# Kernel optimization log

Measured on AMD Instinct MI355X. Metric: run time of the kernel, lower is better.

The kernel has to match this reference:

```python
import jax, jax.numpy as jnp
import numpy as np

N_NODES = 50000
N_EDGES = 800000
IN_C = 128
HID = 128
OUT_C = 64
N_GRAPHS = 256


def setup_inputs() -> dict:
    key = jax.random.key(0)
    ks = jax.random.split(key, 12)
    x = jax.random.normal(ks[0], (N_NODES, IN_C), dtype=jnp.float32)
    edge_index = jax.random.randint(ks[1], (2, N_EDGES), 0, N_NODES, dtype=jnp.int32)
    batch = jnp.sort(jax.random.randint(ks[2], (N_NODES,), 0, N_GRAPHS, dtype=jnp.int32))
    def lin(k, fan_in, fan_out):
        bound = 1.0 / np.sqrt(fan_in)
        kw, kb = jax.random.split(k)
        W = jax.random.uniform(kw, (fan_in, fan_out), minval=-bound, maxval=bound, dtype=jnp.float32)
        b = jax.random.uniform(kb, (fan_out,), minval=-bound, maxval=bound, dtype=jnp.float32)
        return W, b
    W1a, b1a = lin(ks[3], IN_C, HID)
    W1b, b1b = lin(ks[4], HID, HID)
    W2a, b2a = lin(ks[5], HID, HID)
    W2b, b2b = lin(ks[6], HID, HID)
    Wl, bl = lin(ks[7], HID, OUT_C)
    return {"x": x, "edge_index": edge_index, "batch": batch,
            "W1a": W1a, "b1a": b1a, "W1b": W1b, "b1b": b1b,
            "W2a": W2a, "b2a": b2a, "W2b": W2b, "b2b": b2b,
            "Wl": Wl, "bl": bl}


def gin_conv(x, edge_index, Wa, ba, Wb, bb):
    # GINConv with eps=0: h_i = MLP(x_i + sum_{j->i} x_j)
    src, dst = edge_index[0], edge_index[1]
    agg = jax.ops.segment_sum(x[src], dst, num_segments=x.shape[0])  # [N, d]
    h = x + agg
    h = jax.nn.relu(h @ Wa + ba) @ Wb + bb
    return h


def reference(x, edge_index, batch, W1a, b1a, W1b, b1b, W2a, b2a, W2b, b2b, Wl, bl):
    h = gin_conv(x, edge_index, W1a, b1a, W1b, b1b)
    h = gin_conv(h, edge_index, W2a, b2a, W2b, b2b)
    # global mean pool over graphs in the batch
    sums = jax.ops.segment_sum(h, batch, num_segments=N_GRAPHS)          # [G, HID]
    cnts = jax.ops.segment_sum(jnp.ones((h.shape[0],), h.dtype), batch, num_segments=N_GRAPHS)
    pooled = sums / jnp.maximum(cnts, 1.0)[:, None]
    return pooled @ Wl + bl  # [G, OUT_C]
```

## Files before the change

kernel.cpp:

```cpp
#include <hip/hip_runtime.h>

constexpr int N  = 50000;
constexpr int E  = 800000;
constexpr int C  = 128;
constexpr int G  = 256;
constexpr int OC = 64;
constexpr int D  = 64;

constexpr int NBUCK = 196;
constexpr int BCAP  = 5120;
constexpr int EB = (E + 4095) / 4096;
constexpr int WB = 256;
constexpr int XB = (N * C / 8 + 255) / 256;
constexpr int GB = (N + 255) / 256;

typedef __attribute__((ext_vector_type(8))) short short8;
typedef __attribute__((ext_vector_type(4))) float f32x4;
typedef __attribute__((ext_vector_type(2))) float f32x2;

__device__ __forceinline__ unsigned int au(float f) { return __float_as_uint(f); }

__device__ __forceinline__ unsigned short f2bf(float f) {
    unsigned int u = au(f);
    u += 0x7fffu + ((u >> 16) & 1u);
    return (unsigned short)(u >> 16);
}
__device__ __forceinline__ unsigned int pack_bf16(float lo, float hi) {
    return ((au(hi) + 0x8000u) & 0xFFFF0000u) | ((au(lo) + 0x8000u) >> 16);
}

__device__ __forceinline__ void acc16(f32x2* a, uint4 v) {
    a[0] += __builtin_amdgcn_cvt_pk_f32_fp8((int)v.x, false);
    a[1] += __builtin_amdgcn_cvt_pk_f32_fp8((int)v.x, true);
    a[2] += __builtin_amdgcn_cvt_pk_f32_fp8((int)v.y, false);
    a[3] += __builtin_amdgcn_cvt_pk_f32_fp8((int)v.y, true);
    a[4] += __builtin_amdgcn_cvt_pk_f32_fp8((int)v.z, false);
    a[5] += __builtin_amdgcn_cvt_pk_f32_fp8((int)v.z, true);
    a[6] += __builtin_amdgcn_cvt_pk_f32_fp8((int)v.w, false);
    a[7] += __builtin_amdgcn_cvt_pk_f32_fp8((int)v.w, true);
}
__device__ __forceinline__ void set16(f32x2* a, uint4 v) {
    a[0] = __builtin_amdgcn_cvt_pk_f32_fp8((int)v.x, false);
    a[1] = __builtin_amdgcn_cvt_pk_f32_fp8((int)v.x, true);
    a[2] = __builtin_amdgcn_cvt_pk_f32_fp8((int)v.y, false);
    a[3] = __builtin_amdgcn_cvt_pk_f32_fp8((int)v.y, true);
    a[4] = __builtin_amdgcn_cvt_pk_f32_fp8((int)v.z, false);
    a[5] = __builtin_amdgcn_cvt_pk_f32_fp8((int)v.z, true);
    a[6] = __builtin_amdgcn_cvt_pk_f32_fp8((int)v.w, false);
    a[7] = __builtin_amdgcn_cvt_pk_f32_fp8((int)v.w, true);
}


__global__ __launch_bounds__(256) void build_prep_kernel(const int* __restrict__ src,
                                                         const int* __restrict__ dst,
                                                         int* __restrict__ bcount,
                                                         unsigned int* __restrict__ bucketbuf,
                                                         const float* __restrict__ W1a,
                                                         const float* __restrict__ W1b,
                                                         const float* __restrict__ W2a,
                                                         const float* __restrict__ W2b,
                                                         const float* __restrict__ x,
                                                         unsigned short* __restrict__ wt,
                                                         unsigned int* __restrict__ x8,
                                                         const int* __restrict__ batch,
                                                         int* __restrict__ gcnt) {
    int b = blockIdx.x;
    if (b < EB) {
        __shared__ int lcount[NBUCK];
        __shared__ int lbase[NBUCK];
        __shared__ int lcur[NBUCK];
        int tid = threadIdx.x;
        for (int i = tid; i < NBUCK; i += 256) { lcount[i] = 0; lcur[i] = 0; }
        __syncthreads();
        int e0 = b * 4096;
        int sv[16], dv[16];
#pragma unroll
        for (int i = 0; i < 16; ++i) {
            int e = e0 + i * 256 + tid;
            if (e < E) {
                sv[i] = src[e];
                dv[i] = dst[e];
                atomicAdd(&lcount[dv[i] >> 8], 1);
            } else {
                dv[i] = -1;
            }
        }
        __syncthreads();
        if (tid < NBUCK) {
            int c = lcount[tid];
            lbase[tid] = (c > 0) ? atomicAdd(&bcount[tid], c) : 0;
        }
        __syncthreads();
#pragma unroll
        for (int i = 0; i < 16; ++i) {
            if (dv[i] >= 0) {
                int bk = dv[i] >> 8;
                int pos = lbase[bk] + atomicAdd(&lcur[bk], 1);
                if (pos < BCAP)
                    bucketbuf[(size_t)bk * BCAP + pos] =
                        ((unsigned int)sv[i] << 16) | (unsigned int)(dv[i] & 255);
            }
        }
    } else if (b < EB + WB) {
        const float* Ws[4] = {W1a, W1b, W2a, W2b};
        int idx = (b - EB) * 256 + threadIdx.x;
        int which = idx >> 14;
        int el    = idx & 16383;
        int n = el >> 7, k = el & 127;
        wt[idx] = f2bf(Ws[which][k * 128 + n]);
    } else if (b < EB + WB + XB) {
        int idx = (b - EB - WB) * 256 + threadIdx.x;
        const float4* x4 = (const float4*)x;
        float4 v0 = x4[idx * 2];
        float4 v1 = x4[idx * 2 + 1];
        unsigned int lo = 0, hi = 0;
        lo = (unsigned int)__builtin_amdgcn_cvt_pk_fp8_f32(v0.x, v0.y, (int)lo, false);
        lo = (unsigned int)__builtin_amdgcn_cvt_pk_fp8_f32(v0.z, v0.w, (int)lo, true);
        hi = (unsigned int)__builtin_amdgcn_cvt_pk_fp8_f32(v1.x, v1.y, (int)hi, false);
        hi = (unsigned int)__builtin_amdgcn_cvt_pk_fp8_f32(v1.z, v1.w, (int)hi, true);
        ((uint2*)x8)[idx] = make_uint2(lo, hi);
    } else {
        __shared__ int h[G];
        int tid = threadIdx.x;
        h[tid] = 0;
        __syncthreads();
        int i = (b - EB - WB - XB) * 256 + tid;
        if (i < N) atomicAdd(&h[batch[i]], 1);
        __syncthreads();
        int c = h[tid];
        if (c > 0) atomicAdd(&gcnt[tid], c);
    }
}


__global__ __launch_bounds__(256) void bucket_fill_kernel(const int* __restrict__ bcount,
                                                          const unsigned int* __restrict__ bucketbuf,
                                                          unsigned short* __restrict__ ell,
                                                          int* __restrict__ deg) {
    __shared__ int lcur[256];
    int b = blockIdx.x;
    int tid = threadIdx.x;
    lcur[tid] = 0;
    __syncthreads();
    int cnt = min(bcount[b], BCAP);
    const unsigned int* buf = bucketbuf + (size_t)b * BCAP;
    int nbase = b << 8;
    for (int i = tid; i < cnt; i += 256) {
        unsigned int e = buf[i];
        int dlow = (int)(e & 255u);
        int s = (int)(e >> 16);
        int p = atomicAdd(&lcur[dlow], 1);
        if (p < D) ell[(size_t)p * N + nbase + dlow] = (unsigned short)s;
    }
    __syncthreads();
    int node = nbase + tid;
    if (node < N) deg[node] = lcur[tid];
}


__global__ __launch_bounds__(256) void conv_kernel(const unsigned char* __restrict__ Fg,
                                                   const int* __restrict__ deg,
                                                   const unsigned short* __restrict__ ell,
                                                   const unsigned short* __restrict__ WaT,
                                                   const float* __restrict__ ba,
                                                   const unsigned short* __restrict__ WbT,
                                                   const float* __restrict__ bb,
                                                   unsigned char* __restrict__ Hg8,
                                                   const int* __restrict__ batch,
                                                   float* __restrict__ gsum,
                                                   int outFp8) {
    constexpr int LD = 136;
    __shared__ short Xl[64 * LD];
    __shared__ short Wl[128 * LD];
    int tid  = threadIdx.x;
    int lane = tid & 63;
    int wave = tid >> 6;
    int row0 = blockIdx.x * 64;

    const short8* Wa8 = (const short8*)WaT;
#pragma unroll
    for (int i = tid; i < 2048; i += 256) {
        int r = i >> 4, c = i & 15;
        *((short8*)(Wl + r * LD) + c) = Wa8[i];
    }

    {
        int grp = tid >> 3;
        int l   = tid & 7;
        const uint4* F16 = (const uint4*)Fg;
#pragma unroll 1
        for (int pass = 0; pass < 2; ++pass) {
            int lr = pass * 32 + grp;
            int n  = row0 + lr;
            f32x2 a[8];
            if (n < N) {
                int dg = min(deg[n], D);
                const unsigned short* ecol = ell + n;
                set16(a, F16[(size_t)n * 8 + l]);
                int j = 0;
                if (dg >= 8) {
                    int i0 = ecol[0];
                    int i1 = ecol[(size_t)1 * N];
                    int i2 = ecol[(size_t)2 * N];
                    int i3 = ecol[(size_t)3 * N];
                    int i4 = ecol[(size_t)4 * N];
                    int i5 = ecol[(size_t)5 * N];
                    int i6 = ecol[(size_t)6 * N];
                    int i7 = ecol[(size_t)7 * N];
                    uint4 v0 = F16[(size_t)i0 * 8 + l];
                    uint4 v1 = F16[(size_t)i1 * 8 + l];
                    uint4 v2 = F16[(size_t)i2 * 8 + l];
                    uint4 v3 = F16[(size_t)i3 * 8 + l];
                    uint4 v4 = F16[(size_t)i4 * 8 + l];
                    uint4 v5 = F16[(size_t)i5 * 8 + l];
                    uint4 v6 = F16[(size_t)i6 * 8 + l];
                    uint4 v7 = F16[(size_t)i7 * 8 + l];
                    for (j = 8; j + 8 <= dg; j += 8) {
                        int t0 = ecol[(size_t)(j + 0) * N];
                        int t1 = ecol[(size_t)(j + 1) * N];
                        int t2 = ecol[(size_t)(j + 2) * N];
                        int t3 = ecol[(size_t)(j + 3) * N];
                        int t4 = ecol[(size_t)(j + 4) * N];
                        int t5 = ecol[(size_t)(j + 5) * N];
                        int t6 = ecol[(size_t)(j + 6) * N];
                        int t7 = ecol[(size_t)(j + 7) * N];
                        uint4 w0 = F16[(size_t)t0 * 8 + l];
                        uint4 w1 = F16[(size_t)t1 * 8 + l];
                        uint4 w2 = F16[(size_t)t2 * 8 + l];
                        uint4 w3 = F16[(size_t)t3 * 8 + l];
                        uint4 w4 = F16[(size_t)t4 * 8 + l];
                        uint4 w5 = F16[(size_t)t5 * 8 + l];
                        uint4 w6 = F16[(size_t)t6 * 8 + l];
                        uint4 w7 = F16[(size_t)t7 * 8 + l];
                        acc16(a, v0); acc16(a, v1); acc16(a, v2); acc16(a, v3);
                        acc16(a, v4); acc16(a, v5); acc16(a, v6); acc16(a, v7);
                        v0 = w0; v1 = w1; v2 = w2; v3 = w3;
                        v4 = w4; v5 = w5; v6 = w6; v7 = w7;
                    }
                    acc16(a, v0); acc16(a, v1); acc16(a, v2); acc16(a, v3);
                    acc16(a, v4); acc16(a, v5); acc16(a, v6); acc16(a, v7);
                }
                for (; j < dg; ++j) {
                    uint4 v = F16[(size_t)ecol[(size_t)j * N] * 8 + l];
                    acc16(a, v);
                }
            } else {
#pragma unroll
                for (int q = 0; q < 8; ++q) a[q] = (f32x2){0.f, 0.f};
            }
            uint4 o0, o1;
            o0.x = pack_bf16(a[0].x, a[0].y); o0.y = pack_bf16(a[1].x, a[1].y);
            o0.z = pack_bf16(a[2].x, a[2].y); o0.w = pack_bf16(a[3].x, a[3].y);
            o1.x = pack_bf16(a[4].x, a[4].y); o1.y = pack_bf16(a[5].x, a[5].y);
            o1.z = pack_bf16(a[6].x, a[6].y); o1.w = pack_bf16(a[7].x, a[7].y);
            uint4* xp = (uint4*)(Xl + lr * LD + l * 16);
            xp[0] = o0;
            xp[1] = o1;
        }
    }

    int mw = wave >> 1, nw = wave & 1;
    int lid = lane & 15, quad = lane >> 4;

    f32x4 acc[2][4];
#pragma unroll
    for (int nt = 0; nt < 4; ++nt) {
        float b = ba[nw * 64 + nt * 16 + lid];
        acc[0][nt] = (f32x4){b, b, b, b};
        acc[1][nt] = (f32x4){b, b, b, b};
    }
    __syncthreads();

#pragma unroll
    for (int ks = 0; ks < 4; ++ks) {
        short8 a0 = *(const short8*)(Xl + (mw * 32 + lid) * LD + ks * 32 + quad * 8);
        short8 a1 = *(const short8*)(Xl + (mw * 32 + 16 + lid) * LD + ks * 32 + quad * 8);
#pragma unroll
        for (int nt = 0; nt < 4; ++nt) {
            short8 bf = *(const short8*)(Wl + (nw * 64 + nt * 16 + lid) * LD + ks * 32 + quad * 8);
            acc[0][nt] = __builtin_amdgcn_mfma_f32_16x16x32_bf16(a0, bf, acc[0][nt], 0, 0, 0);
            acc[1][nt] = __builtin_amdgcn_mfma_f32_16x16x32_bf16(a1, bf, acc[1][nt], 0, 0, 0);
        }
    }
    __syncthreads();

#pragma unroll
    for (int mt = 0; mt < 2; ++mt) {
#pragma unroll
        for (int nt = 0; nt < 4; ++nt) {
            int mbase = mw * 32 + mt * 16 + quad * 4;
            int n = nw * 64 + nt * 16 + lid;
            f32x4 v = acc[mt][nt];
#pragma unroll
            for (int r = 0; r < 4; ++r)
                Xl[(mbase + r) * LD + n] = (short)f2bf(fmaxf(v[r], 0.f));
        }
    }
    const short8* Wb8 = (const short8*)WbT;
#pragma unroll
    for (int i = tid; i < 2048; i += 256) {
        int r = i >> 4, c = i & 15;
        *((short8*)(Wl + r * LD) + c) = Wb8[i];
    }
    f32x4 acc2[2][4];
#pragma unroll
    for (int nt = 0; nt < 4; ++nt) {
        float b = bb[nw * 64 + nt * 16 + lid];
        acc2[0][nt] = (f32x4){b, b, b, b};
        acc2[1][nt] = (f32x4){b, b, b, b};
    }
    __syncthreads();

#pragma unroll
    for (int ks = 0; ks < 4; ++ks) {
        short8 a0 = *(const short8*)(Xl + (mw * 32 + lid) * LD + ks * 32 + quad * 8);
        short8 a1 = *(const short8*)(Xl + (mw * 32 + 16 + lid) * LD + ks * 32 + quad * 8);
#pragma unroll
        for (int nt = 0; nt < 4; ++nt) {
            short8 bf = *(const short8*)(Wl + (nw * 64 + nt * 16 + lid) * LD + ks * 32 + quad * 8);
            acc2[0][nt] = __builtin_amdgcn_mfma_f32_16x16x32_bf16(a0, bf, acc2[0][nt], 0, 0, 0);
            acc2[1][nt] = __builtin_amdgcn_mfma_f32_16x16x32_bf16(a1, bf, acc2[1][nt], 0, 0, 0);
        }
    }

#pragma unroll
    for (int mt = 0; mt < 2; ++mt) {
#pragma unroll
        for (int nt = 0; nt < 4; ++nt) {
            int mbase = row0 + mw * 32 + mt * 16 + quad * 4;
            int n = nw * 64 + nt * 16 + lid;
            f32x4 v = acc2[mt][nt];
            if (outFp8) {
#pragma unroll
                for (int r = 0; r < 4; ++r) {
                    int row = mbase + r;
                    if (row < N) {
                        unsigned int p = (unsigned int)__builtin_amdgcn_cvt_pk_fp8_f32(v[r], 0.f, 0, false);
                        Hg8[(size_t)row * 128 + n] = (unsigned char)(p & 0xFF);
                    }
                }
            } else {
                int gprev = -1;
                float s = 0.f;
#pragma unroll
                for (int r = 0; r < 4; ++r) {
                    int row = mbase + r;
                    if (row < N) {
                        int g = batch[row];
                        if (g != gprev) {
                            if (gprev >= 0) atomicAdd(&gsum[gprev * C + n], s);
                            gprev = g;
                            s = 0.f;
                        }
                        s += v[r];
                    }
                }
                if (gprev >= 0) atomicAdd(&gsum[gprev * C + n], s);
            }
        }
    }
}


__global__ __launch_bounds__(64) void head_kernel(const float* __restrict__ gsum,
                                                  const int* __restrict__ gcnt,
                                                  const float* __restrict__ Wl,
                                                  const float* __restrict__ bl,
                                                  float* __restrict__ out) {
    int g = blockIdx.x;
    int t = threadIdx.x;
    __shared__ float pooled[C];
    float inv = 1.0f / (float)max(gcnt[g], 1);
    pooled[t]      = gsum[g * C + t] * inv;
    pooled[t + 64] = gsum[g * C + 64 + t] * inv;
    __syncthreads();
    float o = bl[t];
#pragma unroll 4
    for (int k = 0; k < C; ++k) o += pooled[k] * Wl[k * OC + t];
    out[g * OC + t] = o;
}


extern "C" void kernel_launch(void* const* d_in, const int* in_sizes, int n_in,
                              void* d_out, int out_size, void* d_ws, size_t ws_size,
                              hipStream_t stream) {
    const float* x    = (const float*)d_in[0];
    const int*   ei   = (const int*)d_in[1];
    const int*   bat  = (const int*)d_in[2];
    const float* W1a  = (const float*)d_in[3];
    const float* b1a  = (const float*)d_in[4];
    const float* W1b  = (const float*)d_in[5];
    const float* b1b  = (const float*)d_in[6];
    const float* W2a  = (const float*)d_in[7];
    const float* b2a  = (const float*)d_in[8];
    const float* W2b  = (const float*)d_in[9];
    const float* b2b  = (const float*)d_in[10];
    const float* Wl   = (const float*)d_in[11];
    const float* bl   = (const float*)d_in[12];
    float*       out  = (float*)d_out;

    float* gsum    = (float*)d_ws;
    int*   gcnt    = (int*)(gsum + G * C);
    int*   bcount  = gcnt + G;
    int*   deg     = bcount + NBUCK;
    unsigned int* bucketbuf = (unsigned int*)(deg + N);
    unsigned short* ell = (unsigned short*)(bucketbuf + (size_t)NBUCK * BCAP);
    unsigned short* wt  = ell + (size_t)N * D;
    unsigned char*  x8  = (unsigned char*)(wt + 4 * 16384);
    unsigned char*  h8  = x8 + (size_t)N * 128;

    const unsigned short* wt1a = wt;
    const unsigned short* wt1b = wt + 16384;
    const unsigned short* wt2a = wt + 2 * 16384;
    const unsigned short* wt2b = wt + 3 * 16384;

    const int* src = ei;
    const int* dst = ei + E;

    hipMemsetAsync(gsum, 0, (size_t)(G * C + G + NBUCK) * sizeof(int), stream);

    build_prep_kernel<<<EB + WB + XB + GB, 256, 0, stream>>>(src, dst, bcount, bucketbuf,
                                                             W1a, W1b, W2a, W2b, x,
                                                             wt, (unsigned int*)x8,
                                                             bat, gcnt);
    bucket_fill_kernel<<<NBUCK, 256, 0, stream>>>(bcount, bucketbuf, ell, deg);

    int mb = (N + 63) / 64;

    conv_kernel<<<mb, 256, 0, stream>>>(x8, deg, ell, wt1a, b1a, wt1b, b1b,
                                        h8, nullptr, nullptr, 1);
    conv_kernel<<<mb, 256, 0, stream>>>(h8, deg, ell, wt2a, b2a, wt2b, b2b,
                                        nullptr, bat, gsum, 0);

    head_kernel<<<G, 64, 0, stream>>>(gsum, gcnt, Wl, bl, out);
}
```

Measured before the change: 228.0 us.

## Split bucket fill across blocks, halve edges per block, read weights from global

Bucket fill now uses several blocks per bucket and takes slots with global atomics on deg, which is zeroed by the enlarged memset, instead of a shared-memory counter. The edge-bucketing blocks each handle half as many edges, giving more blocks. The conv kernel no longer stages the bf16 weight matrices in LDS; MFMA B operands are read straight from global/L2. The aim is more parallelism in the preprocessing and lower LDS use for occupancy, at the cost of global atomics and uncached-in-LDS weight reads.

```diff
diff --git a/kernel.cpp b/kernel.cpp
--- a/kernel.cpp
+++ b/kernel.cpp
@@ -9,10 +9,12 @@
 
 constexpr int NBUCK = 196;
 constexpr int BCAP  = 5120;
-constexpr int EB = (E + 4095) / 4096;
+constexpr int EPB = 2048;
+constexpr int EB = (E + EPB - 1) / EPB;
 constexpr int WB = 256;
 constexpr int XB = (N * C / 8 + 255) / 256;
 constexpr int GB = (N + 255) / 256;
+constexpr int FSPLIT = 4;
 
 typedef __attribute__((ext_vector_type(8))) short short8;
 typedef __attribute__((ext_vector_type(4))) float f32x4;
@@ -72,10 +74,10 @@
         int tid = threadIdx.x;
         for (int i = tid; i < NBUCK; i += 256) { lcount[i] = 0; lcur[i] = 0; }
         __syncthreads();
-        int e0 = b * 4096;
-        int sv[16], dv[16];
-#pragma unroll
-        for (int i = 0; i < 16; ++i) {
+        int e0 = b * EPB;
+        int sv[8], dv[8];
+#pragma unroll
+        for (int i = 0; i < 8; ++i) {
             int e = e0 + i * 256 + tid;
             if (e < E) {
                 sv[i] = src[e];
@@ -92,7 +94,7 @@
         }
         __syncthreads();
 #pragma unroll
-        for (int i = 0; i < 16; ++i) {
+        for (int i = 0; i < 8; ++i) {
             if (dv[i] >= 0) {
                 int bk = dv[i] >> 8;
                 int pos = lbase[bk] + atomicAdd(&lcur[bk], 1);
@@ -137,24 +139,19 @@
                                                           const unsigned int* __restrict__ bucketbuf,
                                                           unsigned short* __restrict__ ell,
                                                           int* __restrict__ deg) {
-    __shared__ int lcur[256];
-    int b = blockIdx.x;
-    int tid = threadIdx.x;
-    lcur[tid] = 0;
-    __syncthreads();
+    int b = blockIdx.x / FSPLIT;
+    int s = blockIdx.x % FSPLIT;
     int cnt = min(bcount[b], BCAP);
+    int lo = (cnt * s) / FSPLIT;
+    int hi = (cnt * (s + 1)) / FSPLIT;
     const unsigned int* buf = bucketbuf + (size_t)b * BCAP;
     int nbase = b << 8;
-    for (int i = tid; i < cnt; i += 256) {
+    for (int i = lo + (int)threadIdx.x; i < hi; i += 256) {
         unsigned int e = buf[i];
-        int dlow = (int)(e & 255u);
-        int s = (int)(e >> 16);
-        int p = atomicAdd(&lcur[dlow], 1);
-        if (p < D) ell[(size_t)p * N + nbase + dlow] = (unsigned short)s;
-    }
-    __syncthreads();
-    int node = nbase + tid;
-    if (node < N) deg[node] = lcur[tid];
+        int node = nbase + (int)(e & 255u);
+        int p = atomicAdd(&deg[node], 1);
+        if (p < D) ell[(size_t)p * N + node] = (unsigned short)(e >> 16);
+    }
 }
 
 
@@ -171,18 +168,10 @@
                                                    int outFp8) {
     constexpr int LD = 136;
     __shared__ short Xl[64 * LD];
-    __shared__ short Wl[128 * LD];
     int tid  = threadIdx.x;
     int lane = tid & 63;
     int wave = tid >> 6;
     int row0 = blockIdx.x * 64;
-
-    const short8* Wa8 = (const short8*)WaT;
-#pragma unroll
-    for (int i = tid; i < 2048; i += 256) {
-        int r = i >> 4, c = i & 15;
-        *((short8*)(Wl + r * LD) + c) = Wa8[i];
-    }
 
     {
         int grp = tid >> 3;
@@ -277,7 +266,7 @@
         short8 a1 = *(const short8*)(Xl + (mw * 32 + 16 + lid) * LD + ks * 32 + quad * 8);
 #pragma unroll
         for (int nt = 0; nt < 4; ++nt) {
-            short8 bf = *(const short8*)(Wl + (nw * 64 + nt * 16 + lid) * LD + ks * 32 + quad * 8);
+            short8 bf = *(const short8*)(WaT + (nw * 64 + nt * 16 + lid) * 128 + ks * 32 + quad * 8);
             acc[0][nt] = __builtin_amdgcn_mfma_f32_16x16x32_bf16(a0, bf, acc[0][nt], 0, 0, 0);
             acc[1][nt] = __builtin_amdgcn_mfma_f32_16x16x32_bf16(a1, bf, acc[1][nt], 0, 0, 0);
         }
@@ -296,12 +285,6 @@
                 Xl[(mbase + r) * LD + n] = (short)f2bf(fmaxf(v[r], 0.f));
         }
     }
-    const short8* Wb8 = (const short8*)WbT;
-#pragma unroll
-    for (int i = tid; i < 2048; i += 256) {
-        int r = i >> 4, c = i & 15;
-        *((short8*)(Wl + r * LD) + c) = Wb8[i];
-    }
     f32x4 acc2[2][4];
 #pragma unroll
     for (int nt = 0; nt < 4; ++nt) {
@@ -317,7 +300,7 @@
         short8 a1 = *(const short8*)(Xl + (mw * 32 + 16 + lid) * LD + ks * 32 + quad * 8);
 #pragma unroll
         for (int nt = 0; nt < 4; ++nt) {
-            short8 bf = *(const short8*)(Wl + (nw * 64 + nt * 16 + lid) * LD + ks * 32 + quad * 8);
+            short8 bf = *(const short8*)(WbT + (nw * 64 + nt * 16 + lid) * 128 + ks * 32 + quad * 8);
             acc2[0][nt] = __builtin_amdgcn_mfma_f32_16x16x32_bf16(a0, bf, acc2[0][nt], 0, 0, 0);
             acc2[1][nt] = __builtin_amdgcn_mfma_f32_16x16x32_bf16(a1, bf, acc2[1][nt], 0, 0, 0);
         }
@@ -417,13 +400,13 @@
     const int* src = ei;
     const int* dst = ei + E;
 
-    hipMemsetAsync(gsum, 0, (size_t)(G * C + G + NBUCK) * sizeof(int), stream);
+    hipMemsetAsync(gsum, 0, (size_t)(G * C + G + NBUCK + N) * sizeof(int), stream);
 
     build_prep_kernel<<<EB + WB + XB + GB, 256, 0, stream>>>(src, dst, bcount, bucketbuf,
                                                              W1a, W1b, W2a, W2b, x,
                                                              wt, (unsigned int*)x8,
                                                              bat, gcnt);
-    bucket_fill_kernel<<<NBUCK, 256, 0, stream>>>(bcount, bucketbuf, ell, deg);
+    bucket_fill_kernel<<<NBUCK * FSPLIT, 256, 0, stream>>>(bcount, bucketbuf, ell, deg);
 
     int mb = (N + 63) / 64;
 
```

New measurement: 253.5 us. 1.11x slower.

## Switch ELL to row-major with vector index loads and 512-thread conv blocks

Applied to the files above, without the earlier changes.

Changes the neighbour index table from column-major (slot-major) to node-major, so each node's up to 64 neighbour indices sit contiguously and are fetched eight at a time with a single 16-byte load. The conv kernel moves to 512 threads, so each 8-thread group handles one row in a single pass, and the MFMA tiling is split across 8 waves of 32 output columns. Edge bucketing blocks now handle 2048 edges each. In exchange, index writes in bucket_fill become scattered by node rather than coalesced across nodes, and the larger blocks change occupancy and register pressure.

```diff
diff --git a/kernel.cpp b/kernel.cpp
--- a/kernel.cpp
+++ b/kernel.cpp
@@ -9,7 +9,8 @@
 
 constexpr int NBUCK = 196;
 constexpr int BCAP  = 5120;
-constexpr int EB = (E + 4095) / 4096;
+constexpr int EPB = 2048;
+constexpr int EB = (E + EPB - 1) / EPB;
 constexpr int WB = 256;
 constexpr int XB = (N * C / 8 + 255) / 256;
 constexpr int GB = (N + 255) / 256;
@@ -72,10 +73,10 @@
         int tid = threadIdx.x;
         for (int i = tid; i < NBUCK; i += 256) { lcount[i] = 0; lcur[i] = 0; }
         __syncthreads();
-        int e0 = b * 4096;
-        int sv[16], dv[16];
-#pragma unroll
-        for (int i = 0; i < 16; ++i) {
+        int e0 = b * EPB;
+        int sv[8], dv[8];
+#pragma unroll
+        for (int i = 0; i < 8; ++i) {
             int e = e0 + i * 256 + tid;
             if (e < E) {
                 sv[i] = src[e];
@@ -92,7 +93,7 @@
         }
         __syncthreads();
 #pragma unroll
-        for (int i = 0; i < 16; ++i) {
+        for (int i = 0; i < 8; ++i) {
             if (dv[i] >= 0) {
                 int bk = dv[i] >> 8;
                 int pos = lbase[bk] + atomicAdd(&lcur[bk], 1);
@@ -148,9 +149,8 @@
     for (int i = tid; i < cnt; i += 256) {
         unsigned int e = buf[i];
         int dlow = (int)(e & 255u);
-        int s = (int)(e >> 16);
         int p = atomicAdd(&lcur[dlow], 1);
-        if (p < D) ell[(size_t)p * N + nbase + dlow] = (unsigned short)s;
+        if (p < D) ell[(size_t)(nbase + dlow) * D + p] = (unsigned short)(e >> 16);
     }
     __syncthreads();
     int node = nbase + tid;
@@ -158,17 +158,17 @@
 }
 
 
-__global__ __launch_bounds__(256) void conv_kernel(const unsigned char* __restrict__ Fg,
-                                                   const int* __restrict__ deg,
-                                                   const unsigned short* __restrict__ ell,
-                                                   const unsigned short* __restrict__ WaT,
-                                                   const float* __restrict__ ba,
-                                                   const unsigned short* __restrict__ WbT,
-                                                   const float* __restrict__ bb,
-                                                   unsigned char* __restrict__ Hg8,
-                                                   const int* __restrict__ batch,
-                                                   float* __restrict__ gsum,
-                                                   int outFp8) {
+__global__ __launch_bounds__(512, 6) void conv_kernel(const unsigned char* __restrict__ Fg,
+                                                      const int* __restrict__ deg,
+                                                      const unsigned short* __restrict__ ell,
+                                                      const unsigned short* __restrict__ WaT,
+                                                      const float* __restrict__ ba,
+                                                      const unsigned short* __restrict__ WbT,
+                                                      const float* __restrict__ bb,
+                                                      unsigned char* __restrict__ Hg8,
+                                                      const int* __restrict__ batch,
+                                                      float* __restrict__ gsum,
+                                                      int outFp8) {
     constexpr int LD = 136;
     __shared__ short Xl[64 * LD];
     __shared__ short Wl[128 * LD];
@@ -179,7 +179,7 @@
 
     const short8* Wa8 = (const short8*)WaT;
 #pragma unroll
-    for (int i = tid; i < 2048; i += 256) {
+    for (int i = tid; i < 2048; i += 512) {
         int r = i >> 4, c = i & 15;
         *((short8*)(Wl + r * LD) + c) = Wa8[i];
     }
@@ -188,84 +188,86 @@
         int grp = tid >> 3;
         int l   = tid & 7;
         const uint4* F16 = (const uint4*)Fg;
-#pragma unroll 1
-        for (int pass = 0; pass < 2; ++pass) {
-            int lr = pass * 32 + grp;
-            int n  = row0 + lr;
-            f32x2 a[8];
-            if (n < N) {
-                int dg = min(deg[n], D);
-                const unsigned short* ecol = ell + n;
-                set16(a, F16[(size_t)n * 8 + l]);
-                int j = 0;
-                if (dg >= 8) {
-                    int i0 = ecol[0];
-                    int i1 = ecol[(size_t)1 * N];
-                    int i2 = ecol[(size_t)2 * N];
-                    int i3 = ecol[(size_t)3 * N];
-                    int i4 = ecol[(size_t)4 * N];
-                    int i5 = ecol[(size_t)5 * N];
-                    int i6 = ecol[(size_t)6 * N];
-                    int i7 = ecol[(size_t)7 * N];
-                    uint4 v0 = F16[(size_t)i0 * 8 + l];
-                    uint4 v1 = F16[(size_t)i1 * 8 + l];
-                    uint4 v2 = F16[(size_t)i2 * 8 + l];
-                    uint4 v3 = F16[(size_t)i3 * 8 + l];
-                    uint4 v4 = F16[(size_t)i4 * 8 + l];
-                    uint4 v5 = F16[(size_t)i5 * 8 + l];
-                    uint4 v6 = F16[(size_t)i6 * 8 + l];
-                    uint4 v7 = F16[(size_t)i7 * 8 + l];
-                    for (j = 8; j + 8 <= dg; j += 8) {
-                        int t0 = ecol[(size_t)(j + 0) * N];
-                        int t1 = ecol[(size_t)(j + 1) * N];
-                        int t2 = ecol[(size_t)(j + 2) * N];
-                        int t3 = ecol[(size_t)(j + 3) * N];
-                        int t4 = ecol[(size_t)(j + 4) * N];
-                        int t5 = ecol[(size_t)(j + 5) * N];
-                        int t6 = ecol[(size_t)(j + 6) * N];
-                        int t7 = ecol[(size_t)(j + 7) * N];
-                        uint4 w0 = F16[(size_t)t0 * 8 + l];
-                        uint4 w1 = F16[(size_t)t1 * 8 + l];
-                        uint4 w2 = F16[(size_t)t2 * 8 + l];
-                        uint4 w3 = F16[(size_t)t3 * 8 + l];
-                        uint4 w4 = F16[(size_t)t4 * 8 + l];
-                        uint4 w5 = F16[(size_t)t5 * 8 + l];
-                        uint4 w6 = F16[(size_t)t6 * 8 + l];
-                        uint4 w7 = F16[(size_t)t7 * 8 + l];
-                        acc16(a, v0); acc16(a, v1); acc16(a, v2); acc16(a, v3);
-                        acc16(a, v4); acc16(a, v5); acc16(a, v6); acc16(a, v7);
-                        v0 = w0; v1 = w1; v2 = w2; v3 = w3;
-                        v4 = w4; v5 = w5; v6 = w6; v7 = w7;
-                    }
+        int n = row0 + grp;
+        f32x2 a[8];
+        if (n < N) {
+            int dg = min(deg[n], D);
+            const uint4* irow = (const uint4*)(ell + (size_t)n * D);
+            set16(a, F16[(size_t)n * 8 + l]);
+            int nb  = dg >> 3;
+            int rem = dg & 7;
+            if (nb > 0) {
+                uint4 i4 = irow[0];
+                int t0 = (int)(i4.x & 0xffffu), t1 = (int)(i4.x >> 16);
+                int t2 = (int)(i4.y & 0xffffu), t3 = (int)(i4.y >> 16);
+                int t4 = (int)(i4.z & 0xffffu), t5 = (int)(i4.z >> 16);
+                int t6 = (int)(i4.w & 0xffffu), t7 = (int)(i4.w >> 16);
+                uint4 v0 = F16[(size_t)t0 * 8 + l];
+                uint4 v1 = F16[(size_t)t1 * 8 + l];
+                uint4 v2 = F16[(size_t)t2 * 8 + l];
+                uint4 v3 = F16[(size_t)t3 * 8 + l];
+                uint4 v4 = F16[(size_t)t4 * 8 + l];
+                uint4 v5 = F16[(size_t)t5 * 8 + l];
+                uint4 v6 = F16[(size_t)t6 * 8 + l];
+                uint4 v7 = F16[(size_t)t7 * 8 + l];
+                for (int b = 1; b < nb; ++b) {
+                    uint4 j4 = irow[b];
+                    int u0 = (int)(j4.x & 0xffffu), u1 = (int)(j4.x >> 16);
+                    int u2 = (int)(j4.y & 0xffffu), u3 = (int)(j4.y >> 16);
+                    int u4 = (int)(j4.z & 0xffffu), u5 = (int)(j4.z >> 16);
+                    int u6 = (int)(j4.w & 0xffffu), u7 = (int)(j4.w >> 16);
+                    uint4 w0 = F16[(size_t)u0 * 8 + l];
+                    uint4 w1 = F16[(size_t)u1 * 8 + l];
+                    uint4 w2 = F16[(size_t)u2 * 8 + l];
+                    uint4 w3 = F16[(size_t)u3 * 8 + l];
+                    uint4 w4 = F16[(size_t)u4 * 8 + l];
+                    uint4 w5 = F16[(size_t)u5 * 8 + l];
+                    uint4 w6 = F16[(size_t)u6 * 8 + l];
+                    uint4 w7 = F16[(size_t)u7 * 8 + l];
                     acc16(a, v0); acc16(a, v1); acc16(a, v2); acc16(a, v3);
                     acc16(a, v4); acc16(a, v5); acc16(a, v6); acc16(a, v7);
+                    v0 = w0; v1 = w1; v2 = w2; v3 = w3;
+                    v4 = w4; v5 = w5; v6 = w6; v7 = w7;
                 }
-                for (; j < dg; ++j) {
-                    uint4 v = F16[(size_t)ecol[(size_t)j * N] * 8 + l];
-                    acc16(a, v);
+                acc16(a, v0); acc16(a, v1); acc16(a, v2); acc16(a, v3);
+                acc16(a, v4); acc16(a, v5); acc16(a, v6); acc16(a, v7);
+            }
+            if (rem) {
+                uint4 i4 = irow[nb];
+                int t0 = (int)(i4.x & 0xffffu), t1 = (int)(i4.x >> 16);
+                int t2 = (int)(i4.y & 0xffffu), t3 = (int)(i4.y >> 16);
+                int t4 = (int)(i4.z & 0xffffu), t5 = (int)(i4.z >> 16);
+                int t6 = (int)(i4.w & 0xffffu), t7 = (int)(i4.w >> 16);
+                int tv[8] = {t0, t1, t2, t3, t4, t5, t6, t7};
+#pragma unroll
+                for (int m = 0; m < 7; ++m) {
+                    if (m < rem) {
+                        uint4 v = F16[(size_t)tv[m] * 8 + l];
+                        acc16(a, v);
+                    }
                 }
-            } else {
-#pragma unroll
-                for (int q = 0; q < 8; ++q) a[q] = (f32x2){0.f, 0.f};
             }
-            uint4 o0, o1;
-            o0.x = pack_bf16(a[0].x, a[0].y); o0.y = pack_bf16(a[1].x, a[1].y);
-            o0.z = pack_bf16(a[2].x, a[2].y); o0.w = pack_bf16(a[3].x, a[3].y);
-            o1.x = pack_bf16(a[4].x, a[4].y); o1.y = pack_bf16(a[5].x, a[5].y);
-            o1.z = pack_bf16(a[6].x, a[6].y); o1.w = pack_bf16(a[7].x, a[7].y);
-            uint4* xp = (uint4*)(Xl + lr * LD + l * 16);
-            xp[0] = o0;
-            xp[1] = o1;
-        }
-    }
-
-    int mw = wave >> 1, nw = wave & 1;
+        } else {
+#pragma unroll
+            for (int q = 0; q < 8; ++q) a[q] = (f32x2){0.f, 0.f};
+        }
+        uint4 o0, o1;
+        o0.x = pack_bf16(a[0].x, a[0].y); o0.y = pack_bf16(a[1].x, a[1].y);
+        o0.z = pack_bf16(a[2].x, a[2].y); o0.w = pack_bf16(a[3].x, a[3].y);
+        o1.x = pack_bf16(a[4].x, a[4].y); o1.y = pack_bf16(a[5].x, a[5].y);
+        o1.z = pack_bf16(a[6].x, a[6].y); o1.w = pack_bf16(a[7].x, a[7].y);
+        uint4* xp = (uint4*)(Xl + grp * LD + l * 16);
+        xp[0] = o0;
+        xp[1] = o1;
+    }
+
+    int mw = wave >> 2, nw = wave & 3;
     int lid = lane & 15, quad = lane >> 4;
 
-    f32x4 acc[2][4];
-#pragma unroll
-    for (int nt = 0; nt < 4; ++nt) {
-        float b = ba[nw * 64 + nt * 16 + lid];
+    f32x4 acc[2][2];
+#pragma unroll
+    for (int nt = 0; nt < 2; ++nt) {
+        float b = ba[nw * 32 + nt * 16 + lid];
         acc[0][nt] = (f32x4){b, b, b, b};
         acc[1][nt] = (f32x4){b, b, b, b};
     }
@@ -276,8 +278,8 @@
         short8 a0 = *(const short8*)(Xl + (mw * 32 + lid) * LD + ks * 32 + quad * 8);
         short8 a1 = *(const short8*)(Xl + (mw * 32 + 16 + lid) * LD + ks * 32 + quad * 8);
 #pragma unroll
-        for (int nt = 0; nt < 4; ++nt) {
-            short8 bf = *(const short8*)(Wl + (nw * 64 + nt * 16 + lid) * LD + ks * 32 + quad * 8);
+        for (int nt = 0; nt < 2; ++nt) {
+            short8 bf = *(const short8*)(Wl + (nw * 32 + nt * 16 + lid) * LD + ks * 32 + quad * 8);
             acc[0][nt] = __builtin_amdgcn_mfma_f32_16x16x32_bf16(a0, bf, acc[0][nt], 0, 0, 0);
             acc[1][nt] = __builtin_amdgcn_mfma_f32_16x16x32_bf16(a1, bf, acc[1][nt], 0, 0, 0);
         }
@@ -287,9 +289,9 @@
 #pragma unroll
     for (int mt = 0; mt < 2; ++mt) {
 #pragma unroll
-        for (int nt = 0; nt < 4; ++nt) {
+        for (int nt = 0; nt < 2; ++nt) {
             int mbase = mw * 32 + mt * 16 + quad * 4;
-            int n = nw * 64 + nt * 16 + lid;
+            int n = nw * 32 + nt * 16 + lid;
             f32x4 v = acc[mt][nt];
 #pragma unroll
             for (int r = 0; r < 4; ++r)
@@ -298,14 +300,14 @@
     }
     const short8* Wb8 = (const short8*)WbT;
 #pragma unroll
-    for (int i = tid; i < 2048; i += 256) {
+    for (int i = tid; i < 2048; i += 512) {
         int r = i >> 4, c = i & 15;
         *((short8*)(Wl + r * LD) + c) = Wb8[i];
     }
-    f32x4 acc2[2][4];
-#pragma unroll
-    for (int nt = 0; nt < 4; ++nt) {
-        float b = bb[nw * 64 + nt * 16 + lid];
+    f32x4 acc2[2][2];
+#pragma unroll
+    for (int nt = 0; nt < 2; ++nt) {
+        float b = bb[nw * 32 + nt * 16 + lid];
         acc2[0][nt] = (f32x4){b, b, b, b};
         acc2[1][nt] = (f32x4){b, b, b, b};
     }
@@ -316,8 +318,8 @@
         short8 a0 = *(const short8*)(Xl + (mw * 32 + lid) * LD + ks * 32 + quad * 8);
         short8 a1 = *(const short8*)(Xl + (mw * 32 + 16 + lid) * LD + ks * 32 + quad * 8);
 #pragma unroll
-        for (int nt = 0; nt < 4; ++nt) {
-            short8 bf = *(const short8*)(Wl + (nw * 64 + nt * 16 + lid) * LD + ks * 32 + quad * 8);
+        for (int nt = 0; nt < 2; ++nt) {
+            short8 bf = *(const short8*)(Wl + (nw * 32 + nt * 16 + lid) * LD + ks * 32 + quad * 8);
             acc2[0][nt] = __builtin_amdgcn_mfma_f32_16x16x32_bf16(a0, bf, acc2[0][nt], 0, 0, 0);
             acc2[1][nt] = __builtin_amdgcn_mfma_f32_16x16x32_bf16(a1, bf, acc2[1][nt], 0, 0, 0);
         }
@@ -326,9 +328,9 @@
 #pragma unroll
     for (int mt = 0; mt < 2; ++mt) {
 #pragma unroll
-        for (int nt = 0; nt < 4; ++nt) {
+        for (int nt = 0; nt < 2; ++nt) {
             int mbase = row0 + mw * 32 + mt * 16 + quad * 4;
-            int n = nw * 64 + nt * 16 + lid;
+            int n = nw * 32 + nt * 16 + lid;
             f32x4 v = acc2[mt][nt];
             if (outFp8) {
 #pragma unroll
@@ -427,9 +429,9 @@
 
     int mb = (N + 63) / 64;
 
-    conv_kernel<<<mb, 256, 0, stream>>>(x8, deg, ell, wt1a, b1a, wt1b, b1b,
+    conv_kernel<<<mb, 512, 0, stream>>>(x8, deg, ell, wt1a, b1a, wt1b, b1b,
                                         h8, nullptr, nullptr, 1);
-    conv_kernel<<<mb, 256, 0, stream>>>(h8, deg, ell, wt2a, b2a, wt2b, b2b,
+    conv_kernel<<<mb, 512, 0, stream>>>(h8, deg, ell, wt2a, b2a, wt2b, b2b,
                                         nullptr, bat, gsum, 0);
 
     head_kernel<<<G, 64, 0, stream>>>(gsum, gcnt, Wl, bl, out);
```

After: 214.2 us. 1.06x faster.
